# Kernel tuning notes

Measured on AMD Instinct MI355X. Metric: run time of the kernel, lower is better.

The kernel has to match this reference:

```python
import jax, jax.numpy as jnp
import numpy as np
import math

B, S, D, H = 8, 1024, 1024, 16
HD = D // H  # head_features = 64
SCALE = math.sqrt(HD)


def setup_inputs() -> dict:
    key = jax.random.key(0)
    k0, k1, k2, k3, k4 = jax.random.split(key, 5)
    x = jax.random.normal(k0, (B, S, D), dtype=jnp.float32)
    attn_mask = (jax.random.uniform(k1, (B, S, S)) < 0.9).astype(jnp.float32)
    w_scale = 1.0 / math.sqrt(D)  # keep unsafe exp in finite range
    Wq = jax.random.normal(k2, (D, D), dtype=jnp.float32) * w_scale
    Wk = jax.random.normal(k3, (D, D), dtype=jnp.float32) * w_scale
    Wv = jax.random.normal(k4, (D, D), dtype=jnp.float32) * w_scale
    return {"x": x, "attn_mask": attn_mask, "Wq": Wq, "Wk": Wk, "Wv": Wv}


def reference(x, attn_mask, Wq, Wk, Wv):
    b, s, _ = x.shape

    def split_heads(t):  # [b,s,D] -> [b,H,s,HD]
        return t.reshape(b, s, H, HD).transpose(0, 2, 1, 3)

    q = split_heads(x @ Wq)
    k = split_heads(x @ Wk)
    v = split_heads(x @ Wv)

    # unsafe softmax: exp without max subtraction, multiplicative mask, +1e-8 denom
    scores = jnp.einsum('bhsd,bhtd->bhst', q, k) / SCALE
    e = jnp.exp(scores) * attn_mask[:, None, :, :]
    w = e / (e.sum(axis=3, keepdims=True) + 1e-8)

    ctx = jnp.einsum('bhst,bhtd->bhsd', w, v)  # [b,H,s,HD]
    return ctx.transpose(0, 2, 1, 3).reshape(b, s, D)
```

## Files before the change

### kernel.cpp

```cpp
#include <hip/hip_runtime.h>

#define KDIM 1024

typedef _Float16 half8 __attribute__((ext_vector_type(8)));
typedef _Float16 half4 __attribute__((ext_vector_type(4)));
typedef __fp16 fp16x2 __attribute__((ext_vector_type(2)));
typedef __fp16 fp16x4 __attribute__((ext_vector_type(4)));
typedef float f32x4 __attribute__((ext_vector_type(4)));

#if defined(__has_builtin)
#if __has_builtin(__builtin_amdgcn_global_load_lds)
#define HAVE_GLDS 1
#endif
#if __has_builtin(__builtin_amdgcn_exp2f)
#define EXP2(x) __builtin_amdgcn_exp2f(x)
#endif
#if __has_builtin(__builtin_amdgcn_cvt_pkrtz)
#define HAVE_PKRTZ 1
#endif
#if __has_builtin(__builtin_amdgcn_fdot2)
#define HAVE_FDOT2 1
#endif
#endif
#ifndef EXP2
#define EXP2(x) exp2f(x)
#endif

__device__ __forceinline__ void stage16(const _Float16* g, _Float16* wave_base, int lane) {
#ifdef HAVE_GLDS
  __builtin_amdgcn_global_load_lds(
      (const __attribute__((address_space(1))) void*)g,
      (__attribute__((address_space(3))) void*)wave_base, 16, 0, 0);
#else
  *(half8*)(wave_base + lane * 8) = *(const half8*)g;
#endif
}

#define BARRIER() __builtin_amdgcn_s_barrier()
#define LGKM0()                                         \
  do {                                                  \
    asm volatile("s_waitcnt lgkmcnt(0)" ::: "memory");  \
    __builtin_amdgcn_sched_barrier(0);                  \
  } while (0)
#define VMCNT(n)                                               \
  do {                                                         \
    asm volatile("s_waitcnt vmcnt(" #n ")" ::: "memory");      \
  } while (0)

__global__ void prep_kernel(const float* __restrict__ x, const float* __restrict__ am,
                            const float* __restrict__ Wq, const float* __restrict__ Wk,
                            const float* __restrict__ Wv, _Float16* __restrict__ xb,
                            _Float16* __restrict__ Wqkvt, unsigned long long* __restrict__ bits) {
  __shared__ _Float16 tile[32][33];
  int bid = blockIdx.x;
  if (bid < 8192) {
    size_t i = ((size_t)bid * 256 + threadIdx.x) * 4;
    float4 v = *(const float4*)(x + i);
    half4 h = { (_Float16)v.x, (_Float16)v.y, (_Float16)v.z, (_Float16)v.w };
    *(half4*)(xb + i) = h;
  } else if (bid < 11264) {
    int zz = bid - 8192;
    int z = zz >> 10;
    int rem = zz & 1023;
    int bx = rem & 31, by = rem >> 5;
    const float* src = z == 0 ? Wq : (z == 1 ? Wk : Wv);
    _Float16* dst = Wqkvt + (size_t)z * KDIM * KDIM;
    float sc = (z == 0) ? 0.18033688011112042f : 1.0f;
    int tx = threadIdx.x & 31, ty = threadIdx.x >> 5;
    int c0 = bx * 32, r0 = by * 32;
#pragma unroll
    for (int i = 0; i < 4; i++) {
      int r = r0 + ty + i * 8;
      tile[tx][ty + i * 8] = (_Float16)(src[(size_t)r * KDIM + c0 + tx] * sc);
    }
    __syncthreads();
#pragma unroll
    for (int i = 0; i < 4; i++) {
      int n = c0 + ty + i * 8;
      dst[(size_t)n * KDIM + r0 + tx] = tile[ty + i * 8][tx];
    }
  } else {
    size_t i = (size_t)(bid - 11264) * 256 + threadIdx.x;
    unsigned long long b = __ballot(am[i] != 0.0f);
    if ((threadIdx.x & 63) == 0) bits[i >> 6] = b;
  }
}

__global__ __launch_bounds__(512, 2)
void gemm_kernel(const _Float16* __restrict__ A, const _Float16* __restrict__ Bt,
                 _Float16* __restrict__ Qt, _Float16* __restrict__ Kh,
                 _Float16* __restrict__ Vth) {
  __shared__ _Float16 As[2 * 16384];
  __shared__ _Float16 Bs[2 * 16384];
  int tid = threadIdx.x;
  int lane = tid & 63, w = tid >> 6;
  int la = lane & 15, qd = lane >> 4;
  int wm = w & 1, wn = w >> 1;
  int bid = blockIdx.x;
  int wg = (bid & 7) * 48 + (bid >> 3);
  int by = wg / 12, bx = wg - by * 12;
  int m0 = by * 256, n0 = bx * 256;
  int srow = tid >> 3;
  int scc = ((srow & 7) ^ (tid & 7)) << 3;
  const int rc0 = ((qd ^ (la & 7)) << 3);
  const int rc1 = (((4 | qd) ^ (la & 7)) << 3);

  const _Float16* Ab = A + (size_t)m0 * KDIM;
  const _Float16* Bb = Bt + (size_t)n0 * KDIM;

  const _Float16* pA0a = Ab + (size_t)(srow) * KDIM + scc;
  const _Float16* pA0b = Ab + (size_t)(srow + 64) * KDIM + scc;
  const _Float16* pA1a = Ab + (size_t)(srow + 128) * KDIM + scc;
  const _Float16* pA1b = Ab + (size_t)(srow + 192) * KDIM + scc;
  const _Float16* pB0a = Bb + (size_t)(srow) * KDIM + scc;
  const _Float16* pB0b = Bb + (size_t)(srow + 64) * KDIM + scc;
  const _Float16* pB1a = Bb + (size_t)(srow + 128) * KDIM + scc;
  const _Float16* pB1b = Bb + (size_t)(srow + 192) * KDIM + scc;

  _Float16* ldsAw = As + w * 512;
  _Float16* ldsBw = Bs + w * 512;

  const _Float16* baseA0 = As + wm * 4096 + la * 64 + rc0;
  const _Float16* baseA1 = As + wm * 4096 + la * 64 + rc1;
  const _Float16* baseB0 = Bs + wn * 2048 + la * 64 + rc0;
  const _Float16* baseB1 = Bs + wn * 2048 + la * 64 + rc1;

  f32x4 acc[8][4] = {};
  half8 af[4][2], bf0[2][2], bf1[2][2];

#define STAGE_A1(NXT)                                              \
  do {                                                             \
    stage16(pA1a, ldsAw + (NXT) * 16384 + 8192, lane);             \
    stage16(pA1b, ldsAw + (NXT) * 16384 + 8192 + 4096, lane);      \
    pA1a += 64; pA1b += 64;                                        \
  } while (0)
#define STAGE_B1(NXT)                                              \
  do {                                                             \
    stage16(pB1a, ldsBw + (NXT) * 16384 + 8192, lane);             \
    stage16(pB1b, ldsBw + (NXT) * 16384 + 8192 + 4096, lane);      \
    pB1a += 64; pB1b += 64;                                        \
  } while (0)
#define STAGE_A0(CUR)                                              \
  do {                                                             \
    stage16(pA0a, ldsAw + (CUR) * 16384, lane);                    \
    stage16(pA0b, ldsAw + (CUR) * 16384 + 4096, lane);             \
    pA0a += 64; pA0b += 64;                                        \
  } while (0)
#define STAGE_B0(CUR)                                              \
  do {                                                             \
    stage16(pB0a, ldsBw + (CUR) * 16384, lane);                    \
    stage16(pB0b, ldsBw + (CUR) * 16384 + 4096, lane);             \
    pB0a += 64; pB0b += 64;                                        \
  } while (0)
#define LD_AF(CUR, MH)                                                              \
  do {                                                                              \
    _Pragma("unroll") for (int mi = 0; mi < 4; ++mi) {                              \
      af[mi][0] = *(const half8*)(baseA0 + (CUR) * 16384 + (MH) * 8192 + mi * 1024); \
      af[mi][1] = *(const half8*)(baseA1 + (CUR) * 16384 + (MH) * 8192 + mi * 1024); \
    }                                                                               \
  } while (0)
#define LD_BF(BF, CUR, NH)                                                          \
  do {                                                                              \
    _Pragma("unroll") for (int nj = 0; nj < 2; ++nj) {                              \
      BF[nj][0] = *(const half8*)(baseB0 + (CUR) * 16384 + (NH) * 8192 + nj * 1024); \
      BF[nj][1] = *(const half8*)(baseB1 + (CUR) * 16384 + (NH) * 8192 + nj * 1024); \
    }                                                                               \
  } while (0)
#define MFMA_Q(MH, NH, BF)                                                          \
  do {                                                                              \
    __builtin_amdgcn_s_setprio(1);                                                  \
    _Pragma("unroll") for (int mi = 0; mi < 4; ++mi)                                \
        _Pragma("unroll") for (int nj = 0; nj < 2; ++nj) {                          \
      acc[(MH) * 4 + mi][(NH) * 2 + nj] = __builtin_amdgcn_mfma_f32_16x16x32_f16(   \
          af[mi][0], BF[nj][0], acc[(MH) * 4 + mi][(NH) * 2 + nj], 0, 0, 0);        \
      acc[(MH) * 4 + mi][(NH) * 2 + nj] = __builtin_amdgcn_mfma_f32_16x16x32_f16(   \
          af[mi][1], BF[nj][1], acc[(MH) * 4 + mi][(NH) * 2 + nj], 0, 0, 0);        \
    }                                                                               \
    __builtin_amdgcn_s_setprio(0);                                                  \
  } while (0)

  stage16(pA0a, ldsAw, lane);
  stage16(pA0b, ldsAw + 4096, lane);
  stage16(pB0a, ldsBw, lane);
  stage16(pB0b, ldsBw + 4096, lane);
  stage16(pA1a, ldsAw + 8192, lane);
  stage16(pA1b, ldsAw + 8192 + 4096, lane);
  stage16(pB1a, ldsBw + 8192, lane);
  stage16(pB1b, ldsBw + 8192 + 4096, lane);
  stage16(pA0a + 64, ldsAw + 16384, lane);
  stage16(pA0b + 64, ldsAw + 16384 + 4096, lane);
  stage16(pB0a + 64, ldsBw + 16384, lane);
  stage16(pB0b + 64, ldsBw + 16384 + 4096, lane);
  pA0a += 128; pA0b += 128; pB0a += 128; pB0b += 128;
  pA1a += 64;  pA1b += 64;  pB1a += 64;  pB1b += 64;
  VMCNT(8);
  BARRIER();

#define KTILE(T, CUR, NXT)                                     \
  do {                                                         \
    int t = (T);                                               \
                                                  \
    LD_AF(CUR, 0);                                             \
    LD_BF(bf0, CUR, 0);                                        \
    if (t < 15) STAGE_A1(NXT);                                 \
    BARRIER();                                                 \
    LGKM0();                                                   \
    MFMA_Q(0, 0, bf0);                                         \
    if (t < 15) { VMCNT(6); } else { VMCNT(0); }               \
    BARRIER();                                                 \
                                                  \
    LD_BF(bf1, CUR, 1);                                        \
    if (t < 15) STAGE_B1(NXT);                                 \
    BARRIER();                                                 \
    LGKM0();                                                   \
    MFMA_Q(0, 1, bf1);                                         \
    BARRIER();                                                 \
                                                  \
    LD_AF(CUR, 1);                                             \
    if (t < 14) STAGE_A0(CUR);                                 \
    BARRIER();                                                 \
    LGKM0();                                                   \
    MFMA_Q(1, 0, bf0);                                         \
    BARRIER();                                                 \
                                                  \
    if (t < 14) STAGE_B0(CUR);                                 \
    BARRIER();                                                 \
    MFMA_Q(1, 1, bf1);                                         \
    if (t < 14) { VMCNT(8); } else if (t == 14) { VMCNT(4); }  \
    BARRIER();                                                 \
  } while (0)

#pragma unroll 1
  for (int tp = 0; tp < 8; ++tp) {
    KTILE(2 * tp, 0, 1);
    KTILE(2 * tp + 1, 1, 0);
  }

#undef KTILE
#undef MFMA_Q
#undef LD_BF
#undef LD_AF
#undef STAGE_B0
#undef STAGE_A0
#undef STAGE_B1
#undef STAGE_A1

  int which = n0 >> 10;
  int n0k = n0 & 1023;
  if (which == 1) {
#pragma unroll
    for (int mh = 0; mh < 2; ++mh) {
      int srow0 = m0 + mh * 128 + wm * 64;
      int b = srow0 >> 10, s0 = srow0 & 1023;
#pragma unroll
      for (int nh = 0; nh < 2; ++nh)
#pragma unroll
        for (int nj = 0; nj < 2; ++nj) {
          int colh = n0k + nh * 128 + wn * 32 + nj * 16;
          int hh = colh >> 6;
          int d = (colh & 63) + la;
          _Float16* kb = Kh + (size_t)(b * 16 + hh) * 1024 * 64;
#pragma unroll
          for (int mi = 0; mi < 4; ++mi) {
            f32x4 v = acc[mh * 4 + mi][nh * 2 + nj];
            int s = s0 + mi * 16 + qd * 4;
#pragma unroll
            for (int rg = 0; rg < 4; ++rg)
              kb[(size_t)(s + rg) * 64 + d] = (_Float16)v[rg];
          }
        }
    }
  } else {
    _Float16* dst = (which == 0) ? Qt : Vth;
    _Float16* ep = As + w * 1280;
    int rr = lane >> 2, c4 = lane & 3;
#pragma unroll
    for (int mh = 0; mh < 2; ++mh) {
      int srow0 = m0 + mh * 128 + wm * 64;
      int b = srow0 >> 10, s0 = srow0 & 1023;
#pragma unroll
      for (int nh = 0; nh < 2; ++nh)
#pragma unroll
        for (int nj = 0; nj < 2; ++nj) {
          int colh = n0k + nh * 128 + wn * 32 + nj * 16;
          int hh = colh >> 6, d0 = colh & 63;
#pragma unroll
          for (int mi = 0; mi < 4; ++mi) {
            f32x4 v = acc[mh * 4 + mi][nh * 2 + nj];
            half4 hv = { (_Float16)v[0], (_Float16)v[1], (_Float16)v[2], (_Float16)v[3] };
            *(half4*)(ep + la * 72 + mi * 16 + qd * 4) = hv;
          }
          half8 o0 = *(const half8*)(ep + rr * 72 + c4 * 16);
          half8 o1 = *(const half8*)(ep + rr * 72 + c4 * 16 + 8);
          _Float16* gp = dst + ((size_t)(b * 16 + hh) * 64 + d0 + rr) * 1024 + s0 + c4 * 16;
          *(half8*)gp = o0;
          *(half8*)(gp + 8) = o1;
        }
    }
  }
}

__global__ __launch_bounds__(512, 2)
void attn_kernel(const _Float16* __restrict__ Qt, const _Float16* __restrict__ K,
                 const _Float16* __restrict__ Vt, const unsigned long long* __restrict__ mbits,
                 float* __restrict__ out) {
  __shared__ _Float16 Ks[2][2 * 64 * 32];
  __shared__ _Float16 Vs[2][2 * 64 * 40];
  int tid = threadIdx.x;
  int lane = tid & 63, w4 = tid >> 6;
  int la = lane & 15, qd = lane >> 4;
  int linear = blockIdx.x;
  int xlo = linear & 7;
  int tmp = linear >> 3;
  int qt = tmp & 3;
  int hb = (tmp >> 2) * 8 + xlo;
  int h = hb & 15, b = hb >> 4;
  const _Float16* Qp = Qt + (size_t)hb * 64 * 1024;
  const _Float16* Kp = K + (size_t)hb * 1024 * 64;
  const _Float16* Vp = Vt + (size_t)hb * 64 * 1024;
  int q0w = qt * 256 + w4 * 16;
  half8 qf[2][2];
#pragma unroll
  for (int qi = 0; qi < 2; qi++)
#pragma unroll
    for (int ks = 0; ks < 2; ks++)
#pragma unroll
      for (int j = 0; j < 8; j++)
        qf[qi][ks][j] = Qp[(size_t)(ks * 32 + qd * 8 + j) * 1024 + q0w + qi * 128 + la];
  unsigned long long mq[2][4];
#pragma unroll
  for (int qi = 0; qi < 2; qi++) {
    const ulonglong2* mp =
        (const ulonglong2*)(mbits + ((size_t)b * 1024 + q0w + qi * 128 + la) * 16 + qd * 4);
    ulonglong2 m01 = mp[0];
    ulonglong2 m23 = mp[1];
    mq[qi][0] = m01.x; mq[qi][1] = m01.y; mq[qi][2] = m23.x; mq[qi][3] = m23.y;
  }
  f32x4 acco[2][4] = {};
  float rs[2] = {0.f, 0.f};
  int kt_t = (tid & 255) >> 2;
  int kt_d = (tid >> 8) * 32 + (tid & 3) * 8;
  int vd = tid >> 3;
  int vt = (tid & 7) * 8;
  int vs_off = (vt >= 32 ? 2560 : 0) + vd * 40 + (vt & 31);
#if defined(HAVE_FDOT2) && defined(HAVE_PKRTZ)
  fp16x2 one2 = { (__fp16)1.0f, (__fp16)1.0f };
#endif
  {
    stage16(Kp + (size_t)kt_t * 64 + kt_d, Ks[0] + w4 * 512, lane);
    half8 vv = *(const half8*)(Vp + (size_t)vd * 1024 + vt);
    *(half8*)(Vs[0] + vs_off) = vv;
  }
  __syncthreads();
  for (int tt = 0; tt < 16; tt++) {
    int cur = tt & 1, nxt = cur ^ 1;
    half8 vvn;
    if (tt < 15) {
      vvn = *(const half8*)(Vp + (size_t)vd * 1024 + (tt + 1) * 64 + vt);
      stage16(Kp + (size_t)((tt + 1) * 64 + kt_t) * 64 + kt_d, Ks[nxt] + w4 * 512, lane);
    }
    const _Float16* ks_ = Ks[cur];
    const _Float16* vs_ = Vs[cur];
    unsigned long long mw0 = __shfl(mq[0][tt & 3], ((tt >> 2) << 4) + la);
    unsigned long long mw1 = __shfl(mq[1][tt & 3], ((tt >> 2) << 4) + la);
#pragma unroll
    for (int tsub = 0; tsub < 4; tsub++) {
      half8 kf0 = *(const half8*)(ks_ + (tsub * 16 + la) * 32 + qd * 8);
      half8 kf1 = *(const half8*)(ks_ + 2048 + (tsub * 16 + la) * 32 + qd * 8);
      f32x4 a0 = {}, a1 = {};
      a0 = __builtin_amdgcn_mfma_f32_16x16x32_f16(kf0, qf[0][0], a0, 0, 0, 0);
      a1 = __builtin_amdgcn_mfma_f32_16x16x32_f16(kf0, qf[1][0], a1, 0, 0, 0);
      a0 = __builtin_amdgcn_mfma_f32_16x16x32_f16(kf1, qf[0][1], a0, 0, 0, 0);
      a1 = __builtin_amdgcn_mfma_f32_16x16x32_f16(kf1, qf[1][1], a1, 0, 0, 0);
      half4 pf[2];
#pragma unroll
      for (int qi = 0; qi < 2; qi++) {
        const f32x4& aa = qi ? a1 : a0;
        unsigned long long mw = qi ? mw1 : mw0;
        float e0 = ((mw >> (tsub * 16 + qd * 4 + 0)) & 1ull) ? EXP2(aa[0]) : 0.0f;
        float e1 = ((mw >> (tsub * 16 + qd * 4 + 1)) & 1ull) ? EXP2(aa[1]) : 0.0f;
        float e2 = ((mw >> (tsub * 16 + qd * 4 + 2)) & 1ull) ? EXP2(aa[2]) : 0.0f;
        float e3 = ((mw >> (tsub * 16 + qd * 4 + 3)) & 1ull) ? EXP2(aa[3]) : 0.0f;
#ifdef HAVE_PKRTZ
        fp16x2 p01 = __builtin_amdgcn_cvt_pkrtz(e0, e1);
        fp16x2 p23 = __builtin_amdgcn_cvt_pkrtz(e2, e3);
        fp16x4 pfv = __builtin_shufflevector(p01, p23, 0, 1, 2, 3);
        pf[qi] = __builtin_bit_cast(half4, pfv);
#else
        pf[qi][0] = (_Float16)e0; pf[qi][1] = (_Float16)e1;
        pf[qi][2] = (_Float16)e2; pf[qi][3] = (_Float16)e3;
#endif
#if defined(HAVE_FDOT2) && defined(HAVE_PKRTZ)
        rs[qi] = __builtin_amdgcn_fdot2(p01, one2, rs[qi], false);
        rs[qi] = __builtin_amdgcn_fdot2(p23, one2, rs[qi], false);
#else
        rs[qi] += e0 + e1 + e2 + e3;
#endif
      }
#pragma unroll
      for (int nsub = 0; nsub < 4; nsub++) {
        half4 vf = *(const half4*)(vs_ + (tsub >> 1) * 2560 + (nsub * 16 + la) * 40 +
                                   (tsub & 1) * 16 + qd * 4);
        acco[0][nsub] = __builtin_amdgcn_mfma_f32_16x16x16f16(pf[0], vf, acco[0][nsub], 0, 0, 0);
        acco[1][nsub] = __builtin_amdgcn_mfma_f32_16x16x16f16(pf[1], vf, acco[1][nsub], 0, 0, 0);
      }
    }
    if (tt < 15) *(half8*)(Vs[nxt] + vs_off) = vvn;
    __syncthreads();
  }
  float* op = out + (size_t)b * 1024 * 1024 + (size_t)h * 64;
#pragma unroll
  for (int qi = 0; qi < 2; qi++) {
    float r0 = rs[qi];
    r0 += __shfl_xor(r0, 16);
    r0 += __shfl_xor(r0, 32);
    float inv_q = 1.0f / (r0 + 1e-8f);
#pragma unroll
    for (int rg = 0; rg < 4; rg++) {
      float inv = __shfl(inv_q, qd * 4 + rg);
      int s = q0w + qi * 128 + qd * 4 + rg;
#pragma unroll
      for (int nsub = 0; nsub < 4; nsub++)
        op[(size_t)s * 1024 + nsub * 16 + la] = acco[qi][nsub][rg] * inv;
    }
  }
}

extern "C" void kernel_launch(void* const* d_in, const int* in_sizes, int n_in,
                              void* d_out, int out_size, void* d_ws, size_t ws_size,
                              hipStream_t stream) {
  (void)in_sizes; (void)n_in; (void)out_size; (void)ws_size;
  const float* x = (const float*)d_in[0];
  const float* am = (const float*)d_in[1];
  const float* Wq = (const float*)d_in[2];
  const float* Wk = (const float*)d_in[3];
  const float* Wv = (const float*)d_in[4];
  float* out = (float*)d_out;

  char* p = (char*)d_ws;
  _Float16* xb = (_Float16*)p;    p += (size_t)8192 * 1024 * 2;
  _Float16* Wqkvt = (_Float16*)p; p += (size_t)3 * 1024 * 1024 * 2;
  _Float16* Qt = (_Float16*)p;    p += (size_t)8192 * 1024 * 2;
  _Float16* Kh = (_Float16*)p;    p += (size_t)8192 * 1024 * 2;
  _Float16* Vth = (_Float16*)p;   p += (size_t)8192 * 1024 * 2;
  unsigned long long* mb = (unsigned long long*)p;

  prep_kernel<<<44032, 256, 0, stream>>>(x, am, Wq, Wk, Wv, xb, Wqkvt, mb);
  gemm_kernel<<<dim3(384), 512, 0, stream>>>(xb, Wqkvt, Qt, Kh, Vth);
  attn_kernel<<<512, 512, 0, stream>>>(Qt, Kh, Vth, mb, out);
}
```

Measured before the change: 253.7 us.

## Retile QKV GEMM to 256x192 tiles with 512 blocks; swizzle K tile in LDS

Changes the QKV projection GEMM tile from 256x256 to 256x192. That gives 512 workgroups instead of 384, which maps more evenly onto the CU count, and it reduces LDS for B. The stage/MFMA pipeline and the epilogue are restructured so each 16-column subtile picks its Q/K/V destination independently. The attention kernel also adds an XOR swizzle on the K tile in LDS to reduce bank conflicts on fragment reads. Risks: a smaller N tile lowers arithmetic intensity per block, and the prefetch schedule is shallower.

```diff
diff --git a/kernel.cpp b/kernel.cpp
--- a/kernel.cpp
+++ b/kernel.cpp
@@ -91,15 +91,15 @@
                  _Float16* __restrict__ Qt, _Float16* __restrict__ Kh,
                  _Float16* __restrict__ Vth) {
   __shared__ _Float16 As[2 * 16384];
-  __shared__ _Float16 Bs[2 * 16384];
+  __shared__ _Float16 Bs[2 * 12288];
   int tid = threadIdx.x;
   int lane = tid & 63, w = tid >> 6;
   int la = lane & 15, qd = lane >> 4;
   int wm = w & 1, wn = w >> 1;
   int bid = blockIdx.x;
-  int wg = (bid & 7) * 48 + (bid >> 3);
-  int by = wg / 12, bx = wg - by * 12;
-  int m0 = by * 256, n0 = bx * 256;
+  int wg = (bid & 7) * 64 + (bid >> 3);
+  int by = wg >> 4, bx = wg & 15;
+  int m0 = by * 256, n0 = bx * 192;
   int srow = tid >> 3;
   int scc = ((srow & 7) ^ (tid & 7)) << 3;
   const int rc0 = ((qd ^ (la & 7)) << 3);
@@ -112,88 +112,63 @@
   const _Float16* pA0b = Ab + (size_t)(srow + 64) * KDIM + scc;
   const _Float16* pA1a = Ab + (size_t)(srow + 128) * KDIM + scc;
   const _Float16* pA1b = Ab + (size_t)(srow + 192) * KDIM + scc;
-  const _Float16* pB0a = Bb + (size_t)(srow) * KDIM + scc;
-  const _Float16* pB0b = Bb + (size_t)(srow + 64) * KDIM + scc;
-  const _Float16* pB1a = Bb + (size_t)(srow + 128) * KDIM + scc;
-  const _Float16* pB1b = Bb + (size_t)(srow + 192) * KDIM + scc;
+  const _Float16* pB0 = Bb + (size_t)(srow) * KDIM + scc;
+  const _Float16* pB1 = Bb + (size_t)(srow + 64) * KDIM + scc;
+  const _Float16* pB2 = Bb + (size_t)(srow + 128) * KDIM + scc;
 
   _Float16* ldsAw = As + w * 512;
   _Float16* ldsBw = Bs + w * 512;
 
   const _Float16* baseA0 = As + wm * 4096 + la * 64 + rc0;
   const _Float16* baseA1 = As + wm * 4096 + la * 64 + rc1;
-  const _Float16* baseB0 = Bs + wn * 2048 + la * 64 + rc0;
-  const _Float16* baseB1 = Bs + wn * 2048 + la * 64 + rc1;
-
-  f32x4 acc[8][4] = {};
-  half8 af[4][2], bf0[2][2], bf1[2][2];
-
-#define STAGE_A1(NXT)                                              \
-  do {                                                             \
-    stage16(pA1a, ldsAw + (NXT) * 16384 + 8192, lane);             \
-    stage16(pA1b, ldsAw + (NXT) * 16384 + 8192 + 4096, lane);      \
-    pA1a += 64; pA1b += 64;                                        \
-  } while (0)
-#define STAGE_B1(NXT)                                              \
-  do {                                                             \
-    stage16(pB1a, ldsBw + (NXT) * 16384 + 8192, lane);             \
-    stage16(pB1b, ldsBw + (NXT) * 16384 + 8192 + 4096, lane);      \
-    pB1a += 64; pB1b += 64;                                        \
-  } while (0)
-#define STAGE_A0(CUR)                                              \
-  do {                                                             \
-    stage16(pA0a, ldsAw + (CUR) * 16384, lane);                    \
-    stage16(pA0b, ldsAw + (CUR) * 16384 + 4096, lane);             \
-    pA0a += 64; pA0b += 64;                                        \
-  } while (0)
-#define STAGE_B0(CUR)                                              \
-  do {                                                             \
-    stage16(pB0a, ldsBw + (CUR) * 16384, lane);                    \
-    stage16(pB0b, ldsBw + (CUR) * 16384 + 4096, lane);             \
-    pB0a += 64; pB0b += 64;                                        \
-  } while (0)
-#define LD_AF(CUR, MH)                                                              \
+  const _Float16* baseB0 = Bs + (wn * 16 + la) * 64 + rc0;
+  const _Float16* baseB1 = Bs + (wn * 16 + la) * 64 + rc1;
+
+  f32x4 acc[8][3] = {};
+  half8 af[4][2], bf0[2], bf1[2], bf2[2];
+
+#define STAGE_A0(B)                                       \
+  do {                                                    \
+    stage16(pA0a, ldsAw + (B) * 16384, lane);             \
+    stage16(pA0b, ldsAw + (B) * 16384 + 4096, lane);      \
+    pA0a += 64; pA0b += 64;                               \
+  } while (0)
+#define STAGE_A1(B)                                       \
+  do {                                                    \
+    stage16(pA1a, ldsAw + (B) * 16384 + 8192, lane);      \
+    stage16(pA1b, ldsAw + (B) * 16384 + 12288, lane);     \
+    pA1a += 64; pA1b += 64;                               \
+  } while (0)
+#define STAGE_B0(B)                                       \
+  do { stage16(pB0, ldsBw + (B) * 12288, lane); pB0 += 64; } while (0)
+#define STAGE_B1(B)                                       \
+  do { stage16(pB1, ldsBw + (B) * 12288 + 4096, lane); pB1 += 64; } while (0)
+#define STAGE_B2(B)                                       \
+  do { stage16(pB2, ldsBw + (B) * 12288 + 8192, lane); pB2 += 64; } while (0)
+#define LD_AF(CUR, MH)                                                               \
+  do {                                                                               \
+    _Pragma("unroll") for (int mi = 0; mi < 4; ++mi) {                               \
+      af[mi][0] = *(const half8*)(baseA0 + (CUR) * 16384 + (MH) * 8192 + mi * 1024); \
+      af[mi][1] = *(const half8*)(baseA1 + (CUR) * 16384 + (MH) * 8192 + mi * 1024); \
+    }                                                                                \
+  } while (0)
+#define LD_B(BF, CUR, NJ)                                                  \
+  do {                                                                     \
+    BF[0] = *(const half8*)(baseB0 + (CUR) * 12288 + (NJ) * 4096);         \
+    BF[1] = *(const half8*)(baseB1 + (CUR) * 12288 + (NJ) * 4096);         \
+  } while (0)
+#define MFMA_N(MH, NJ, BF)                                                          \
   do {                                                                              \
     _Pragma("unroll") for (int mi = 0; mi < 4; ++mi) {                              \
-      af[mi][0] = *(const half8*)(baseA0 + (CUR) * 16384 + (MH) * 8192 + mi * 1024); \
-      af[mi][1] = *(const half8*)(baseA1 + (CUR) * 16384 + (MH) * 8192 + mi * 1024); \
+      acc[(MH) * 4 + mi][NJ] = __builtin_amdgcn_mfma_f32_16x16x32_f16(              \
+          af[mi][0], BF[0], acc[(MH) * 4 + mi][NJ], 0, 0, 0);                       \
+      acc[(MH) * 4 + mi][NJ] = __builtin_amdgcn_mfma_f32_16x16x32_f16(              \
+          af[mi][1], BF[1], acc[(MH) * 4 + mi][NJ], 0, 0, 0);                       \
     }                                                                               \
   } while (0)
-#define LD_BF(BF, CUR, NH)                                                          \
-  do {                                                                              \
-    _Pragma("unroll") for (int nj = 0; nj < 2; ++nj) {                              \
-      BF[nj][0] = *(const half8*)(baseB0 + (CUR) * 16384 + (NH) * 8192 + nj * 1024); \
-      BF[nj][1] = *(const half8*)(baseB1 + (CUR) * 16384 + (NH) * 8192 + nj * 1024); \
-    }                                                                               \
-  } while (0)
-#define MFMA_Q(MH, NH, BF)                                                          \
-  do {                                                                              \
-    __builtin_amdgcn_s_setprio(1);                                                  \
-    _Pragma("unroll") for (int mi = 0; mi < 4; ++mi)                                \
-        _Pragma("unroll") for (int nj = 0; nj < 2; ++nj) {                          \
-      acc[(MH) * 4 + mi][(NH) * 2 + nj] = __builtin_amdgcn_mfma_f32_16x16x32_f16(   \
-          af[mi][0], BF[nj][0], acc[(MH) * 4 + mi][(NH) * 2 + nj], 0, 0, 0);        \
-      acc[(MH) * 4 + mi][(NH) * 2 + nj] = __builtin_amdgcn_mfma_f32_16x16x32_f16(   \
-          af[mi][1], BF[nj][1], acc[(MH) * 4 + mi][(NH) * 2 + nj], 0, 0, 0);        \
-    }                                                                               \
-    __builtin_amdgcn_s_setprio(0);                                                  \
-  } while (0)
-
-  stage16(pA0a, ldsAw, lane);
-  stage16(pA0b, ldsAw + 4096, lane);
-  stage16(pB0a, ldsBw, lane);
-  stage16(pB0b, ldsBw + 4096, lane);
-  stage16(pA1a, ldsAw + 8192, lane);
-  stage16(pA1b, ldsAw + 8192 + 4096, lane);
-  stage16(pB1a, ldsBw + 8192, lane);
-  stage16(pB1b, ldsBw + 8192 + 4096, lane);
-  stage16(pA0a + 64, ldsAw + 16384, lane);
-  stage16(pA0b + 64, ldsAw + 16384 + 4096, lane);
-  stage16(pB0a + 64, ldsBw + 16384, lane);
-  stage16(pB0b + 64, ldsBw + 16384 + 4096, lane);
-  pA0a += 128; pA0b += 128; pB0a += 128; pB0b += 128;
-  pA1a += 64;  pA1b += 64;  pB1a += 64;  pB1b += 64;
-  VMCNT(8);
+
+  STAGE_A0(0); STAGE_B0(0); STAGE_A1(0); STAGE_B1(0); STAGE_B2(0);
+  VMCNT(0);
   BARRIER();
 
 #define KTILE(T, CUR, NXT)                                     \
@@ -201,32 +176,37 @@
     int t = (T);                                               \
                                                   \
     LD_AF(CUR, 0);                                             \
-    LD_BF(bf0, CUR, 0);                                        \
+    LD_B(bf0, CUR, 0);                                         \
+    if (t < 15) { STAGE_A0(NXT); STAGE_B0(NXT); }              \
+    BARRIER();                                                 \
+    LGKM0();                                                   \
+    __builtin_amdgcn_s_setprio(1);                             \
+    MFMA_N(0, 0, bf0);                                         \
+    __builtin_amdgcn_s_setprio(0);                             \
+    if (t < 15) { VMCNT(3); } else { VMCNT(0); }               \
+    BARRIER();                                                 \
+                                                  \
+    LD_B(bf1, CUR, 1);                                         \
+    LD_B(bf2, CUR, 2);                                         \
     if (t < 15) STAGE_A1(NXT);                                 \
     BARRIER();                                                 \
     LGKM0();                                                   \
-    MFMA_Q(0, 0, bf0);                                         \
-    if (t < 15) { VMCNT(6); } else { VMCNT(0); }               \
-    BARRIER();                                                 \
-                                                  \
-    LD_BF(bf1, CUR, 1);                                        \
-    if (t < 15) STAGE_B1(NXT);                                 \
-    BARRIER();                                                 \
-    LGKM0();                                                   \
-    MFMA_Q(0, 1, bf1);                                         \
+    __builtin_amdgcn_s_setprio(1);                             \
+    MFMA_N(0, 1, bf1);                                         \
+    MFMA_N(0, 2, bf2);                                         \
+    __builtin_amdgcn_s_setprio(0);                             \
     BARRIER();                                                 \
                                                   \
     LD_AF(CUR, 1);                                             \
-    if (t < 14) STAGE_A0(CUR);                                 \
+    if (t < 15) { STAGE_B1(NXT); STAGE_B2(NXT); }              \
     BARRIER();                                                 \
     LGKM0();                                                   \
-    MFMA_Q(1, 0, bf0);                                         \
-    BARRIER();                                                 \
-                                                  \
-    if (t < 14) STAGE_B0(CUR);                                 \
-    BARRIER();                                                 \
-    MFMA_Q(1, 1, bf1);                                         \
-    if (t < 14) { VMCNT(8); } else if (t == 14) { VMCNT(4); }  \
+    __builtin_amdgcn_s_setprio(1);                             \
+    MFMA_N(1, 0, bf0);                                         \
+    MFMA_N(1, 1, bf1);                                         \
+    MFMA_N(1, 2, bf2);                                         \
+    __builtin_amdgcn_s_setprio(0);                             \
+    if (t < 15) { VMCNT(4); }                                  \
     BARRIER();                                                 \
   } while (0)
 
@@ -237,65 +217,51 @@
   }
 
 #undef KTILE
-#undef MFMA_Q
-#undef LD_BF
+#undef MFMA_N
+#undef LD_B
 #undef LD_AF
+#undef STAGE_B2
+#undef STAGE_B1
 #undef STAGE_B0
+#undef STAGE_A1
 #undef STAGE_A0
-#undef STAGE_B1
-#undef STAGE_A1
-
-  int which = n0 >> 10;
-  int n0k = n0 & 1023;
-  if (which == 1) {
-#pragma unroll
-    for (int mh = 0; mh < 2; ++mh) {
-      int srow0 = m0 + mh * 128 + wm * 64;
-      int b = srow0 >> 10, s0 = srow0 & 1023;
-#pragma unroll
-      for (int nh = 0; nh < 2; ++nh)
-#pragma unroll
-        for (int nj = 0; nj < 2; ++nj) {
-          int colh = n0k + nh * 128 + wn * 32 + nj * 16;
-          int hh = colh >> 6;
-          int d = (colh & 63) + la;
-          _Float16* kb = Kh + (size_t)(b * 16 + hh) * 1024 * 64;
-#pragma unroll
-          for (int mi = 0; mi < 4; ++mi) {
-            f32x4 v = acc[mh * 4 + mi][nh * 2 + nj];
-            int s = s0 + mi * 16 + qd * 4;
-#pragma unroll
-            for (int rg = 0; rg < 4; ++rg)
-              kb[(size_t)(s + rg) * 64 + d] = (_Float16)v[rg];
-          }
+
+  int rr = lane >> 2, c4 = lane & 3;
+  _Float16* ep = As + w * 1280;
+#pragma unroll
+  for (int mh = 0; mh < 2; ++mh) {
+    int srow0 = m0 + mh * 128 + wm * 64;
+    int b = srow0 >> 10, s0 = srow0 & 1023;
+#pragma unroll
+    for (int nj = 0; nj < 3; ++nj) {
+      int colh = n0 + wn * 16 + nj * 64;
+      int whichf = colh >> 10;
+      int cm = colh & 1023;
+      int hh = cm >> 6, d0 = cm & 63;
+      if (whichf == 1) {
+        _Float16* kb = Kh + (size_t)(b * 16 + hh) * 1024 * 64;
+#pragma unroll
+        for (int mi = 0; mi < 4; ++mi) {
+          f32x4 v = acc[mh * 4 + mi][nj];
+          int s = s0 + mi * 16 + qd * 4;
+#pragma unroll
+          for (int rg = 0; rg < 4; ++rg)
+            kb[(size_t)(s + rg) * 64 + d0 + la] = (_Float16)v[rg];
         }
-    }
-  } else {
-    _Float16* dst = (which == 0) ? Qt : Vth;
-    _Float16* ep = As + w * 1280;
-    int rr = lane >> 2, c4 = lane & 3;
-#pragma unroll
-    for (int mh = 0; mh < 2; ++mh) {
-      int srow0 = m0 + mh * 128 + wm * 64;
-      int b = srow0 >> 10, s0 = srow0 & 1023;
-#pragma unroll
-      for (int nh = 0; nh < 2; ++nh)
-#pragma unroll
-        for (int nj = 0; nj < 2; ++nj) {
-          int colh = n0k + nh * 128 + wn * 32 + nj * 16;
-          int hh = colh >> 6, d0 = colh & 63;
-#pragma unroll
-          for (int mi = 0; mi < 4; ++mi) {
-            f32x4 v = acc[mh * 4 + mi][nh * 2 + nj];
-            half4 hv = { (_Float16)v[0], (_Float16)v[1], (_Float16)v[2], (_Float16)v[3] };
-            *(half4*)(ep + la * 72 + mi * 16 + qd * 4) = hv;
-          }
-          half8 o0 = *(const half8*)(ep + rr * 72 + c4 * 16);
-          half8 o1 = *(const half8*)(ep + rr * 72 + c4 * 16 + 8);
-          _Float16* gp = dst + ((size_t)(b * 16 + hh) * 64 + d0 + rr) * 1024 + s0 + c4 * 16;
-          *(half8*)gp = o0;
-          *(half8*)(gp + 8) = o1;
+      } else {
+        _Float16* dst = (whichf == 0) ? Qt : Vth;
+#pragma unroll
+        for (int mi = 0; mi < 4; ++mi) {
+          f32x4 v = acc[mh * 4 + mi][nj];
+          half4 hv = { (_Float16)v[0], (_Float16)v[1], (_Float16)v[2], (_Float16)v[3] };
+          *(half4*)(ep + la * 72 + mi * 16 + qd * 4) = hv;
         }
+        half8 o0 = *(const half8*)(ep + rr * 72 + c4 * 16);
+        half8 o1 = *(const half8*)(ep + rr * 72 + c4 * 16 + 8);
+        _Float16* gp = dst + ((size_t)(b * 16 + hh) * 64 + d0 + rr) * 1024 + s0 + c4 * 16;
+        *(half8*)gp = o0;
+        *(half8*)(gp + 8) = o1;
+      }
     }
   }
 }
@@ -339,7 +305,8 @@
   f32x4 acco[2][4] = {};
   float rs[2] = {0.f, 0.f};
   int kt_t = (tid & 255) >> 2;
-  int kt_d = (tid >> 8) * 32 + (tid & 3) * 8;
+  int kt_d = (tid >> 8) * 32 + (((tid & 3) ^ ((tid >> 2) & 3) ^ ((tid >> 4) & 3)) << 3);
+  int kc8 = ((qd ^ (la & 3) ^ (la >> 2)) << 3);
   int vd = tid >> 3;
   int vt = (tid & 7) * 8;
   int vs_off = (vt >= 32 ? 2560 : 0) + vd * 40 + (vt & 31);
@@ -365,8 +332,8 @@
     unsigned long long mw1 = __shfl(mq[1][tt & 3], ((tt >> 2) << 4) + la);
 #pragma unroll
     for (int tsub = 0; tsub < 4; tsub++) {
-      half8 kf0 = *(const half8*)(ks_ + (tsub * 16 + la) * 32 + qd * 8);
-      half8 kf1 = *(const half8*)(ks_ + 2048 + (tsub * 16 + la) * 32 + qd * 8);
+      half8 kf0 = *(const half8*)(ks_ + (tsub * 16 + la) * 32 + kc8);
+      half8 kf1 = *(const half8*)(ks_ + 2048 + (tsub * 16 + la) * 32 + kc8);
       f32x4 a0 = {}, a1 = {};
       a0 = __builtin_amdgcn_mfma_f32_16x16x32_f16(kf0, qf[0][0], a0, 0, 0, 0);
       a1 = __builtin_amdgcn_mfma_f32_16x16x32_f16(kf0, qf[1][0], a1, 0, 0, 0);
@@ -446,6 +413,6 @@
   unsigned long long* mb = (unsigned long long*)p;
 
   prep_kernel<<<44032, 256, 0, stream>>>(x, am, Wq, Wk, Wv, xb, Wqkvt, mb);
-  gemm_kernel<<<dim3(384), 512, 0, stream>>>(xb, Wqkvt, Qt, Kh, Vth);
+  gemm_kernel<<<dim3(512), 512, 0, stream>>>(xb, Wqkvt, Qt, Kh, Vth);
   attn_kernel<<<512, 512, 0, stream>>>(Qt, Kh, Vth, mb, out);
 }
```

Measured after the change: 249.8 us. About the same (-1.5%).
